# Optimization experiments

Measured on AMD Instinct MI355X. Metric: run time of the kernel, lower is better.

## Reference

```python
import jax, jax.numpy as jnp
import numpy as np

N, H, W, M = 1, 128, 128, 16
HID, STY, CIN, NC, COL = 256, 256, 128, 7, 64


def _lrelu(v):
    return jnp.where(v > 0, v, 0.2 * v)


def _conv(x, w, b=None):
    y = jax.lax.conv_general_dilated(x, w, (1, 1), 'SAME',
                                     dimension_numbers=('NCHW', 'OIHW', 'NCHW'))
    return y if b is None else y + b[None, :, None, None]


def _modlin(f, z, Wt, Wa, ba, Wb, bb):
    # ModLinear, bias=False, mod_bias=True, output_mode=True:
    # y = (f * alpha) @ W^T + beta
    alpha = z @ Wa.T + ba          # [N, in]
    beta = z @ Wb.T + bb           # [N, out]
    return jnp.einsum('nsi,oi->nso', f * alpha[:, None, :], Wt) + beta[:, None, :]


def setup_inputs() -> dict:
    key = jax.random.key(0)
    k = jax.random.split(key, 24)
    s = lambda f: np.float32(1.0 / np.sqrt(f))
    inp = {}
    inp['x'] = jax.random.normal(k[0], (N, H, W, M, CIN), jnp.float32)
    inp['m'] = jax.random.uniform(k[1], (N, H, W, M, NC), jnp.float32)
    inp['z'] = jax.random.normal(k[2], (N, STY), jnp.float32)
    inp['dists'] = jax.random.uniform(k[3], (N, H, W, M), jnp.float32) * 0.05
    # RenderMLP params
    inp['w1'] = jax.random.normal(k[4], (HID, CIN)) * s(CIN)
    inp['b1'] = jnp.zeros((HID,), jnp.float32)
    inp['wma'] = jax.random.normal(k[5], (HID, NC)) * s(NC)
    # 5 stacked ModLinears (fc_2, fc_3, fc_4, fc_5, fc_6)
    inp['ml_w'] = jax.random.normal(k[6], (5, HID, HID)) * s(HID)
    inp['ml_wa'] = jax.random.normal(k[7], (5, HID, STY)) * s(STY)
    inp['ml_ba'] = jnp.ones((5, HID), jnp.float32)
    inp['ml_wb'] = jax.random.normal(k[8], (5, HID, STY)) * s(STY)
    inp['ml_bb'] = jnp.zeros((5, HID), jnp.float32)
    inp['wsig'] = jax.random.normal(k[9], (1, HID)) * s(HID)
    inp['bsig'] = jnp.zeros((1,), jnp.float32)
    inp['wc'] = jax.random.normal(k[10], (COL, HID)) * s(HID)
    inp['bc'] = jnp.zeros((COL,), jnp.float32)
    # RenderCNN params
    inp['wz'] = jax.random.normal(k[11], (4 * HID, STY)) * s(STY)
    inp['bz'] = jnp.zeros((4 * HID,), jnp.float32)
    inp['c1_w'] = jax.random.normal(k[12], (HID, COL, 1, 1)) * s(COL)
    inp['c1_b'] = jnp.zeros((HID,), jnp.float32)
    inp['c2a_w'] = jax.random.normal(k[13], (HID, HID, 3, 3)) * s(HID * 9)
    inp['c2a_b'] = jnp.zeros((HID,), jnp.float32)
    inp['c2b_w'] = jax.random.normal(k[14], (HID, HID, 3, 3)) * s(HID * 9)
    inp['c3a_w'] = jax.random.normal(k[15], (HID, HID, 3, 3)) * s(HID * 9)
    inp['c3a_b'] = jnp.zeros((HID,), jnp.float32)
    inp['c3b_w'] = jax.random.normal(k[16], (HID, HID, 3, 3)) * s(HID * 9)
    inp['c4a_w'] = jax.random.normal(k[17], (HID, HID, 1, 1)) * s(HID)
    inp['c4a_b'] = jnp.zeros((HID,), jnp.float32)
    inp['c4b_w'] = jax.random.normal(k[18], (HID, HID, 1, 1)) * s(HID)
    inp['c4b_b'] = jnp.zeros((HID,), jnp.float32)
    inp['c4_w'] = jax.random.normal(k[19], (3, HID, 1, 1)) * s(HID)
    inp['c4_b'] = jnp.zeros((3,), jnp.float32)
    return inp


def reference(x, m, z, dists, w1, b1, wma, ml_w, ml_wa, ml_ba, ml_wb, ml_bb,
              wsig, bsig, wc, bc, wz, bz, c1_w, c1_b, c2a_w, c2a_b, c2b_w,
              c3a_w, c3a_b, c3b_w, c4a_w, c4a_b, c4b_w, c4b_b, c4_w, c4_b):
    n, h, w_, mm, cin = x.shape
    xf = x.reshape(n, -1, cin)              # [N, S, 128], S = H*W*M
    mf = m.reshape(n, -1, m.shape[-1])      # [N, S, 7]
    # RenderMLP
    f = jnp.einsum('nsi,oi->nso', xf, w1) + b1 + jnp.einsum('nsi,oi->nso', mf, wma)
    f = _lrelu(f)
    for i in range(3):  # fc_2, fc_3, fc_4
        f = _lrelu(_modlin(f, z, ml_w[i], ml_wa[i], ml_ba[i], ml_wb[i], ml_bb[i]))
    sigma = jnp.einsum('nsi,oi->nso', f, wsig) + bsig   # [N, S, 1]
    for i in (3, 4):    # fc_5, fc_6
        f = _lrelu(_modlin(f, z, ml_w[i], ml_wa[i], ml_ba[i], ml_wb[i], ml_bb[i]))
    c = jnp.einsum('nsi,oi->nso', f, wc) + bc           # [N, S, 64]
    # Volumetric alpha compositing along the M ray samples
    sigma = sigma.reshape(n, h, w_, mm)
    c = c.reshape(n, h, w_, mm, -1)
    alpha = 1.0 - jnp.exp(-jax.nn.relu(sigma) * dists)  # [N,H,W,M]
    t = jnp.cumprod(1.0 - alpha + 1e-10, axis=-1)
    t_excl = jnp.concatenate([jnp.ones_like(t[..., :1]), t[..., :-1]], axis=-1)
    wgt = alpha * t_excl
    feat = jnp.einsum('nhwm,nhwmc->nchw', wgt, c)       # [N, 64, H, W]
    # RenderCNN with style modulation
    zc = z @ wz.T + bz
    a0, a1, a2, a3 = jnp.split(zc, 4, axis=-1)
    mod = lambda y, wm, bm: y * (wm[:, :, None, None] + 1.0) + bm[:, :, None, None]
    y = _lrelu(_conv(feat, c1_w, c1_b))
    y = y + _conv(_lrelu(_conv(y, c2a_w, c2a_b)), c2b_w)
    y = _lrelu(mod(y, a0, a1))
    y = y + _conv(_lrelu(_conv(y, c3a_w, c3a_b)), c3b_w)
    y = _lrelu(mod(y, a2, a3))
    y = y + _conv(_lrelu(_conv(y, c4a_w, c4a_b)), c4b_w, c4b_b)
    y = _lrelu(y)
    return _conv(y, c4_w, c4_b)  # [N, 3, H, W]
```

## Files before the change

### kernel.cpp

```cpp
#include <hip/hip_runtime.h>
#include <hip/hip_bf16.h>

#define NPIX 16384
#define S_TOT 262144

typedef __attribute__((ext_vector_type(8))) short bf16x8;
typedef __attribute__((ext_vector_type(4))) float f32x4;

__device__ __forceinline__ float lrelu(float v) { return v > 0.f ? v : 0.2f * v; }
__device__ __forceinline__ unsigned short f2b(float f) {
  unsigned u = __float_as_uint(f);
  return (unsigned short)((u + 0x7FFFu + ((u >> 16) & 1u)) >> 16);
}
__device__ __forceinline__ unsigned pk2(float a, float b) {
  return (unsigned)f2b(a) | ((unsigned)f2b(b) << 16);
}
__device__ __forceinline__ float b2f(short s) {
  return __uint_as_float(((unsigned)(unsigned short)s) << 16);
}
__device__ __forceinline__ float f_lo(int u) { return __uint_as_float((unsigned)u << 16); }
__device__ __forceinline__ float f_hi(int u) { return __uint_as_float((unsigned)u & 0xffff0000u); }

__device__ float g_alpha[5 * 256];
__device__ float g_beta[5 * 256];
__device__ float g_amod[1024];
__device__ float g_sigma[S_TOT];
__device__ float g_c[S_TOT * 64];
__device__ short g_featb[NPIX * 64];
__device__ short g_y1[NPIX * 256];
__device__ short g_y2[NPIX * 256];
__device__ short g_y3[NPIX * 256];
__device__ short g_t [NPIX * 256];
__device__ short g_wpack[385024];
#define O_C1  0
#define O_C2A 16384
#define O_C2B (16384 + 589824)
#define O_C3A (16384 + 2 * 589824)
#define O_C3B (16384 + 3 * 589824)
#define O_C4A (16384 + 4 * 589824)
#define O_C4B (16384 + 4 * 589824 + 65536)
__device__ short g_wpack2[2506752];

__global__ __launch_bounds__(256) void kparams(const float* __restrict__ z,
    const float* __restrict__ wa, const float* __restrict__ ba,
    const float* __restrict__ wb, const float* __restrict__ bb,
    const float* __restrict__ wz, const float* __restrict__ bz) {
  __shared__ float zs[256];
  const int t = threadIdx.x;
  zs[t] = z[t];
  __syncthreads();
  for (int l = 0; l < 5; ++l) {
    float accA = ba[l * 256 + t];
    float accB = bb[l * 256 + t];
    const float* rowA = wa + (l * 256 + t) * 256;
    const float* rowB = wb + (l * 256 + t) * 256;
    for (int k = 0; k < 256; k += 4) {
      float4 va = *(const float4*)(rowA + k);
      float4 vb = *(const float4*)(rowB + k);
      accA += va.x * zs[k] + va.y * zs[k + 1] + va.z * zs[k + 2] + va.w * zs[k + 3];
      accB += vb.x * zs[k] + vb.y * zs[k + 1] + vb.z * zs[k + 2] + vb.w * zs[k + 3];
    }
    g_alpha[l * 256 + t] = accA;
    g_beta[l * 256 + t] = accB;
  }
  for (int j = t; j < 1024; j += 256) {
    float acc = bz[j];
    const float* row = wz + j * 256;
    for (int k = 0; k < 256; k += 4) {
      float4 v = *(const float4*)(row + k);
      acc += v.x * zs[k] + v.y * zs[k + 1] + v.z * zs[k + 2] + v.w * zs[k + 3];
    }
    g_amod[j] = acc;
  }
}

__global__ __launch_bounds__(256) void kprep(
    const float* __restrict__ w1, const float* __restrict__ wma,
    const float* __restrict__ mlw, const float* __restrict__ wc) {
  const int idx = blockIdx.x * 256 + threadIdx.x;
  float val;
  if (idx < 40960) {
    int mt = idx / 2560, r2 = idx % 2560;
    int ks = r2 / 512, r = r2 % 512;
    int ln = r >> 3, j = r & 7;
    int oc = mt * 16 + (ln & 15);
    int k = ks * 32 + (ln >> 4) * 8 + j;
    val = (k < 128) ? w1[oc * 128 + k] : ((k < 135) ? wma[oc * 7 + (k - 128)] : 0.f);
  } else if (idx < 368640) {
    int t = idx - 40960;
    int l = t / 65536, t2 = t % 65536;
    int mt = t2 / 4096, r2 = t2 % 4096;
    int ks = r2 / 512, r = r2 % 512;
    int ln = r >> 3, j = r & 7;
    int oc = mt * 16 + (ln & 15);
    int k = ks * 32 + (ln >> 4) * 8 + j;
    val = mlw[l * 65536 + oc * 256 + k] * g_alpha[l * 256 + k];
  } else {
    int t = idx - 368640;
    int mt = t / 4096, r2 = t % 4096;
    int ks = r2 / 512, r = r2 % 512;
    int ln = r >> 3, j = r & 7;
    int oc = mt * 16 + (ln & 15);
    int k = ks * 32 + (ln >> 4) * 8 + j;
    val = wc[oc * 256 + k];
  }
  g_wpack[idx] = (short)f2b(val);
}

__global__ __launch_bounds__(256) void kprep_cnn(
    const float* __restrict__ c1w,
    const float* __restrict__ c2aw, const float* __restrict__ c2bw,
    const float* __restrict__ c3aw, const float* __restrict__ c3bw,
    const float* __restrict__ c4aw, const float* __restrict__ c4bw) {
  const int idx = blockIdx.x * 256 + threadIdx.x;
  float val;
  if (idx < 16384) {
    int mt = idx / 1024, r2 = idx % 1024;
    int ks = r2 / 512, r = r2 % 512;
    int ln = r >> 3, j = r & 7;
    int oc = mt * 16 + (ln & 15);
    int k = ks * 32 + (ln >> 4) * 8 + j;
    val = c1w[oc * 64 + k];
  } else if (idx < O_C4A) {
    int t = idx - 16384;
    int cv = t / 589824, t2 = t % 589824;
    const float* w = (cv == 0) ? c2aw : (cv == 1) ? c2bw : (cv == 2) ? c3aw : c3bw;
    int mt = t2 / 36864, r2 = t2 % 36864;
    int ks = r2 / 512, r = r2 % 512;
    int ln = r >> 3, j = r & 7;
    int oc = mt * 16 + (ln & 15);
    int k = ks * 32 + (ln >> 4) * 8 + j;
    int tap = k >> 8, ic = k & 255;
    val = w[oc * 2304 + ic * 9 + tap];
  } else {
    int t = idx - O_C4A;
    const float* w = (t < 65536) ? c4aw : c4bw;
    int t2 = t & 65535;
    int mt = t2 / 4096, r2 = t2 % 4096;
    int ks = r2 / 512, r = r2 % 512;
    int ln = r >> 3, j = r & 7;
    int oc = mt * 16 + (ln & 15);
    int k = ks * 32 + (ln >> 4) * 8 + j;
    val = w[oc * 256 + k];
  }
  g_wpack2[idx] = (short)f2b(val);
}

__device__ __forceinline__ bf16x8 ldsB(const short* buf, int s, int kbyte) {
  const char* p = (const char*)buf + s * 512 + (kbyte ^ ((s & 7) << 4));
  return *(const bf16x8*)p;
}

template<int KS>
__device__ __forceinline__ void layer_gemm(const short* __restrict__ gA,
    const short* __restrict__ inb, short* __restrict__ outb,
    const float* __restrict__ bias, int lane, int w) {
  const f32x4 zero = {0.f, 0.f, 0.f, 0.f};
  f32x4 acc[4][4];
#pragma unroll
  for (int mi = 0; mi < 4; ++mi)
#pragma unroll
    for (int ni = 0; ni < 4; ++ni) acc[mi][ni] = zero;
  const int lrow = lane & 15;
  const int lkb = (lane >> 4) * 16;
#pragma unroll
  for (int ks = 0; ks < KS; ++ks) {
    bf16x8 A[4], B[4];
#pragma unroll
    for (int mi = 0; mi < 4; ++mi)
      A[mi] = *(const bf16x8*)(gA + (size_t)((w * 4 + mi) * KS + ks) * 512 + lane * 8);
#pragma unroll
    for (int ni = 0; ni < 4; ++ni)
      B[ni] = ldsB(inb, ni * 16 + lrow, ks * 64 + lkb);
#pragma unroll
    for (int mi = 0; mi < 4; ++mi)
#pragma unroll
      for (int ni = 0; ni < 4; ++ni)
        acc[mi][ni] = __builtin_amdgcn_mfma_f32_16x16x32_bf16(A[mi], B[ni], acc[mi][ni], 0, 0, 0);
  }
  const int rb = (lane >> 4) * 4;
#pragma unroll
  for (int mi = 0; mi < 4; ++mi) {
    const int oc0 = w * 64 + mi * 16 + rb;
    const float b0 = bias[oc0], b1 = bias[oc0 + 1], b2 = bias[oc0 + 2], b3 = bias[oc0 + 3];
#pragma unroll
    for (int ni = 0; ni < 4; ++ni) {
      const int s = ni * 16 + lrow;
      f32x4 a = acc[mi][ni];
      float v0 = lrelu(a[0] + b0), v1 = lrelu(a[1] + b1);
      float v2 = lrelu(a[2] + b2), v3 = lrelu(a[3] + b3);
      char* p = (char*)outb + s * 512 + ((oc0 * 2) ^ ((s & 7) << 4));
      *(int2*)p = make_int2((int)pk2(v0, v1), (int)pk2(v2, v3));
    }
  }
}

__global__ __launch_bounds__(256, 2) void kmlp_mfma(
    const float* __restrict__ x, const float* __restrict__ m_in,
    const float* __restrict__ b1, const float* __restrict__ bc,
    const float* __restrict__ wsig, const float* __restrict__ bsig) {
  __shared__ short fbuf[2][16384];
  __shared__ float bias_all[1600];
  __shared__ float wsig_lds[256];
  __shared__ float sred[256];
  const int tid = threadIdx.x;
  const int lane = tid & 63, w = tid >> 6;
  const int s0 = blockIdx.x * 64;

  {
    const float* xp = x + (size_t)s0 * 128;
    const int s = tid >> 2, c = tid & 3;
#pragma unroll
    for (int e = 0; e < 4; ++e) {
      float4 f0 = *(const float4*)(xp + s * 128 + c * 32 + e * 8);
      float4 f1 = *(const float4*)(xp + s * 128 + c * 32 + e * 8 + 4);
      int4 pk;
      pk.x = (int)pk2(f0.x, f0.y); pk.y = (int)pk2(f0.z, f0.w);
      pk.z = (int)pk2(f1.x, f1.y); pk.w = (int)pk2(f1.z, f1.w);
      char* p = (char*)fbuf[0] + s * 512 + ((c * 64 + e * 16) ^ ((s & 7) << 4));
      *(int4*)p = pk;
    }
  }
  if (tid < 64) {
    const float* mp = m_in + (size_t)(s0 + tid) * 7;
    float mv[8];
#pragma unroll
    for (int q = 0; q < 7; ++q) mv[q] = mp[q];
    mv[7] = 0.f;
    int4 pk;
    pk.x = (int)pk2(mv[0], mv[1]); pk.y = (int)pk2(mv[2], mv[3]);
    pk.z = (int)pk2(mv[4], mv[5]); pk.w = (int)pk2(mv[6], mv[7]);
    char* base = (char*)fbuf[0] + tid * 512;
    const int swz = (tid & 7) << 4;
    *(int4*)(base + (256 ^ swz)) = pk;
    int4 zz = make_int4(0, 0, 0, 0);
    *(int4*)(base + (272 ^ swz)) = zz;
    *(int4*)(base + (288 ^ swz)) = zz;
    *(int4*)(base + (304 ^ swz)) = zz;
  }
  bias_all[tid] = b1[tid];
  for (int i = tid; i < 1280; i += 256) bias_all[256 + i] = g_beta[i];
  if (tid < 64) bias_all[1536 + tid] = bc[tid];
  wsig_lds[tid] = wsig[tid];
  __syncthreads();

  layer_gemm<5>(g_wpack,                     fbuf[0], fbuf[1], bias_all,        lane, w);
  __syncthreads();
  layer_gemm<8>(g_wpack + 40960,             fbuf[1], fbuf[0], bias_all + 256,  lane, w);
  __syncthreads();
  layer_gemm<8>(g_wpack + 40960 + 65536,     fbuf[0], fbuf[1], bias_all + 512,  lane, w);
  __syncthreads();
  layer_gemm<8>(g_wpack + 40960 + 2 * 65536, fbuf[1], fbuf[0], bias_all + 768,  lane, w);
  __syncthreads();
  {
    const int s = tid & 63, q = tid >> 6;
    float part = 0.f;
#pragma unroll
    for (int e = 0; e < 8; ++e) {
      bf16x8 v = ldsB(fbuf[0], s, q * 128 + e * 16);
      const float* wp = wsig_lds + q * 64 + e * 8;
#pragma unroll
      for (int j = 0; j < 8; ++j) part += b2f(v[j]) * wp[j];
    }
    sred[q * 64 + s] = part;
  }
  __syncthreads();
  if (tid < 64)
    g_sigma[s0 + tid] = sred[tid] + sred[64 + tid] + sred[128 + tid] + sred[192 + tid] + bsig[0];
  layer_gemm<8>(g_wpack + 40960 + 3 * 65536, fbuf[0], fbuf[1], bias_all + 1024, lane, w);
  __syncthreads();
  layer_gemm<8>(g_wpack + 40960 + 4 * 65536, fbuf[1], fbuf[0], bias_all + 1280, lane, w);
  __syncthreads();
  {
    const f32x4 zero = {0.f, 0.f, 0.f, 0.f};
    f32x4 acc[4] = {zero, zero, zero, zero};
    const int lrow = lane & 15, lkb = (lane >> 4) * 16;
    const short* gA = g_wpack + 368640;
#pragma unroll
    for (int ks = 0; ks < 8; ++ks) {
      bf16x8 A = *(const bf16x8*)(gA + (size_t)(w * 8 + ks) * 512 + lane * 8);
#pragma unroll
      for (int ni = 0; ni < 4; ++ni) {
        bf16x8 B = ldsB(fbuf[0], ni * 16 + lrow, ks * 64 + lkb);
        acc[ni] = __builtin_amdgcn_mfma_f32_16x16x32_bf16(A, B, acc[ni], 0, 0, 0);
      }
    }
    const int rb = (lane >> 4) * 4;
    const int oc0 = w * 16 + rb;
    const float b0 = bias_all[1536 + oc0], b1v = bias_all[1537 + oc0];
    const float b2v = bias_all[1538 + oc0], b3 = bias_all[1539 + oc0];
#pragma unroll
    for (int ni = 0; ni < 4; ++ni) {
      const int s = ni * 16 + lrow;
      float4 vv;
      vv.x = acc[ni][0] + b0; vv.y = acc[ni][1] + b1v;
      vv.z = acc[ni][2] + b2v; vv.w = acc[ni][3] + b3;
      *(float4*)(g_c + (size_t)(s0 + s) * 64 + oc0) = vv;
    }
  }
}

__global__ __launch_bounds__(256) void kcomposite(const float* __restrict__ dists) {
  const int tid = threadIdx.x;
  const int p = blockIdx.x * 4 + (tid >> 6);
  const int ch = tid & 63;
  const int base = p * 16;
  float T = 1.f, acc = 0.f;
  for (int mm = 0; mm < 16; ++mm) {
    float sgm = g_sigma[base + mm];
    float d = dists[base + mm];
    float a = 1.f - expf(-fmaxf(sgm, 0.f) * d);
    acc += a * T * g_c[(size_t)(base + mm) * 64 + ch];
    T *= (1.f - a + 1e-10f);
  }
  g_featb[p * 64 + ch] = (short)f2b(acc);
}

template<int IC>
__global__ __launch_bounds__(256, 2) void kgemm1x1(const short* __restrict__ in,
    const short* __restrict__ gA, const float* __restrict__ bias,
    const short* __restrict__ res, int domod, const float* __restrict__ modAB,
    short* __restrict__ out) {
  constexpr int KS = IC / 32;
  constexpr int ROWB = IC * 2;
  __shared__ short binb[32 * IC];
  const int tid = threadIdx.x;
  const int lane = tid & 63, w = tid >> 6;
  const int px0 = blockIdx.x * 32;

  for (int e = tid; e < 32 * IC / 8; e += 256) {
    const int px = e / (IC / 8), lg = e % (IC / 8);
    bf16x8 v = *(const bf16x8*)(in + (size_t)(px0 + px) * IC + lg * 8);
    char* p = (char*)binb + px * ROWB + ((lg * 16) ^ ((px & 7) << 4));
    *(bf16x8*)p = v;
  }
  __syncthreads();

  const f32x4 zero = {0.f, 0.f, 0.f, 0.f};
  f32x4 acc[4][2];
#pragma unroll
  for (int mi = 0; mi < 4; ++mi)
#pragma unroll
    for (int ni = 0; ni < 2; ++ni) acc[mi][ni] = zero;
  const int lrow = lane & 15;
  const int lkb = (lane >> 4) * 16;
#pragma unroll
  for (int ks = 0; ks < KS; ++ks) {
    bf16x8 A[4], B[2];
#pragma unroll
    for (int mi = 0; mi < 4; ++mi)
      A[mi] = *(const bf16x8*)(gA + (size_t)((w * 4 + mi) * KS + ks) * 512 + lane * 8);
#pragma unroll
    for (int ni = 0; ni < 2; ++ni) {
      const int s = ni * 16 + lrow;
      const char* p = (const char*)binb + s * ROWB + ((ks * 64 + lkb) ^ ((s & 7) << 4));
      B[ni] = *(const bf16x8*)p;
    }
#pragma unroll
    for (int mi = 0; mi < 4; ++mi)
#pragma unroll
      for (int ni = 0; ni < 2; ++ni)
        acc[mi][ni] = __builtin_amdgcn_mfma_f32_16x16x32_bf16(A[mi], B[ni], acc[mi][ni], 0, 0, 0);
  }
  const int rb = (lane >> 4) * 4;
#pragma unroll
  for (int mi = 0; mi < 4; ++mi) {
    const int oc = w * 64 + mi * 16 + rb;
    float bv[4] = {0.f, 0.f, 0.f, 0.f};
    if (bias) { bv[0] = bias[oc]; bv[1] = bias[oc + 1]; bv[2] = bias[oc + 2]; bv[3] = bias[oc + 3]; }
#pragma unroll
    for (int ni = 0; ni < 2; ++ni) {
      const int gpx = px0 + ni * 16 + lrow;
      f32x4 a = acc[mi][ni];
      float v[4];
#pragma unroll
      for (int r = 0; r < 4; ++r) v[r] = a[r] + bv[r];
      if (res) {
        int2 rv = *(const int2*)(res + (size_t)gpx * 256 + oc);
        v[0] += f_lo(rv.x); v[1] += f_hi(rv.x); v[2] += f_lo(rv.y); v[3] += f_hi(rv.y);
      }
      if (domod) {
#pragma unroll
        for (int r = 0; r < 4; ++r) v[r] = v[r] * (modAB[oc + r] + 1.f) + modAB[256 + oc + r];
      }
#pragma unroll
      for (int r = 0; r < 4; ++r) v[r] = lrelu(v[r]);
      *(int2*)(out + (size_t)gpx * 256 + oc) = make_int2((int)pk2(v[0], v[1]), (int)pk2(v[2], v[3]));
    }
  }
}

__global__ __launch_bounds__(256, 2) void kconv3(const short* __restrict__ in,
    const short* __restrict__ gA, const float* __restrict__ bias,
    const short* __restrict__ res, int domod, const float* __restrict__ modAB,
    short* __restrict__ out) {
  __shared__ short halo[136 * 64];
  const int tid = threadIdx.x;
  const int lane = tid & 63, w = tid >> 6;
  const int oct = blockIdx.x >> 8;
  const int pxt = blockIdx.x & 255;
  const int x0 = (pxt & 3) * 32, y0 = (pxt >> 2) * 2;
  const int oc0 = oct * 128 + w * 32;
  const int lrow = lane & 15;
  const int lkb = (lane >> 4) * 16;

  const f32x4 zero = {0.f, 0.f, 0.f, 0.f};
  f32x4 acc[2][4];
#pragma unroll
  for (int mi = 0; mi < 2; ++mi)
#pragma unroll
    for (int ni = 0; ni < 4; ++ni) acc[mi][ni] = zero;

#pragma unroll 1
  for (int c = 0; c < 4; ++c) {
    for (int e = tid; e < 1088; e += 256) {
      const int row = e >> 3, lg = e & 7;
      const int yy = row / 34, xx = row - yy * 34;
      const int gy = y0 - 1 + yy, gx = x0 - 1 + xx;
      bf16x8 v = {0, 0, 0, 0, 0, 0, 0, 0};
      if (gy >= 0 && gy < 128 && gx >= 0 && gx < 128)
        v = *(const bf16x8*)(in + (size_t)((gy << 7) + gx) * 256 + c * 64 + lg * 8);
      char* p = (char*)halo + row * 128 + ((lg * 16) ^ ((row & 7) << 4));
      *(bf16x8*)p = v;
    }
    __syncthreads();
#pragma unroll
    for (int tap = 0; tap < 9; ++tap) {
      const int ky = tap / 3, kx = tap - ky * 3;
#pragma unroll
      for (int s = 0; s < 2; ++s) {
        const int ksg = tap * 8 + c * 2 + s;
        bf16x8 A[2], B[4];
#pragma unroll
        for (int mi = 0; mi < 2; ++mi)
          A[mi] = *(const bf16x8*)(gA + (size_t)(((oct * 8 + w * 2 + mi) * 72 + ksg)) * 512 + lane * 8);
#pragma unroll
        for (int ni = 0; ni < 4; ++ni) {
          const int p = ni * 16 + lrow;
          const int row = ((p >> 5) + ky) * 34 + (p & 31) + kx;
          const char* bp = (const char*)halo + row * 128 + ((s * 64 + lkb) ^ ((row & 7) << 4));
          B[ni] = *(const bf16x8*)bp;
        }
#pragma unroll
        for (int mi = 0; mi < 2; ++mi)
#pragma unroll
          for (int ni = 0; ni < 4; ++ni)
            acc[mi][ni] = __builtin_amdgcn_mfma_f32_16x16x32_bf16(A[mi], B[ni], acc[mi][ni], 0, 0, 0);
      }
    }
    __syncthreads();
  }

  const int rb = (lane >> 4) * 4;
#pragma unroll
  for (int mi = 0; mi < 2; ++mi) {
    const int oc = oc0 + mi * 16 + rb;
    float bv[4] = {0.f, 0.f, 0.f, 0.f};
    if (bias) { bv[0] = bias[oc]; bv[1] = bias[oc + 1]; bv[2] = bias[oc + 2]; bv[3] = bias[oc + 3]; }
#pragma unroll
    for (int ni = 0; ni < 4; ++ni) {
      const int p = ni * 16 + lrow;
      const int gpx = (y0 + (p >> 5)) * 128 + x0 + (p & 31);
      f32x4 a = acc[mi][ni];
      float v[4];
#pragma unroll
      for (int r = 0; r < 4; ++r) v[r] = a[r] + bv[r];
      if (res) {
        int2 rv = *(const int2*)(res + (size_t)gpx * 256 + oc);
        v[0] += f_lo(rv.x); v[1] += f_hi(rv.x); v[2] += f_lo(rv.y); v[3] += f_hi(rv.y);
      }
      if (domod) {
#pragma unroll
        for (int r = 0; r < 4; ++r) v[r] = v[r] * (modAB[oc + r] + 1.f) + modAB[256 + oc + r];
      }
#pragma unroll
      for (int r = 0; r < 4; ++r) v[r] = lrelu(v[r]);
      *(int2*)(out + (size_t)gpx * 256 + oc) = make_int2((int)pk2(v[0], v[1]), (int)pk2(v[2], v[3]));
    }
  }
}

__global__ __launch_bounds__(256) void kfinal(const short* __restrict__ in,
    const float* __restrict__ w, const float* __restrict__ bias, float* __restrict__ outp) {
  __shared__ float wl[768];
  const int tid = threadIdx.x;
  for (int i = tid; i < 768; i += 256) wl[i] = w[i];
  __syncthreads();
  const int lane = tid & 63;
  const int px = blockIdx.x * 8 + (tid >> 6) * 2 + (lane >> 5);
  const int j = lane & 31;
  bf16x8 v = *(const bf16x8*)(in + (size_t)px * 256 + j * 8);
  float s0 = 0.f, s1 = 0.f, s2 = 0.f;
#pragma unroll
  for (int q = 0; q < 8; ++q) {
    float f = b2f(v[q]);
    s0 += f * wl[j * 8 + q];
    s1 += f * wl[256 + j * 8 + q];
    s2 += f * wl[512 + j * 8 + q];
  }
#pragma unroll
  for (int off = 1; off < 32; off <<= 1) {
    s0 += __shfl_xor(s0, off);
    s1 += __shfl_xor(s1, off);
    s2 += __shfl_xor(s2, off);
  }
  if (j == 0) {
    outp[px] = s0 + bias[0];
    outp[NPIX + px] = s1 + bias[1];
    outp[2 * NPIX + px] = s2 + bias[2];
  }
}

extern "C" void kernel_launch(void* const* d_in, const int* in_sizes, int n_in,
                              void* d_out, int out_size, void* d_ws, size_t ws_size,
                              hipStream_t stream) {
  (void)in_sizes; (void)n_in; (void)out_size; (void)d_ws; (void)ws_size;
  const float* x    = (const float*)d_in[0];
  const float* m    = (const float*)d_in[1];
  const float* z    = (const float*)d_in[2];
  const float* dists= (const float*)d_in[3];
  const float* w1   = (const float*)d_in[4];
  const float* b1   = (const float*)d_in[5];
  const float* wma  = (const float*)d_in[6];
  const float* mlw  = (const float*)d_in[7];
  const float* mlwa = (const float*)d_in[8];
  const float* mlba = (const float*)d_in[9];
  const float* mlwb = (const float*)d_in[10];
  const float* mlbb = (const float*)d_in[11];
  const float* wsig = (const float*)d_in[12];
  const float* bsig = (const float*)d_in[13];
  const float* wc   = (const float*)d_in[14];
  const float* bc   = (const float*)d_in[15];
  const float* wz   = (const float*)d_in[16];
  const float* bz   = (const float*)d_in[17];
  const float* c1w  = (const float*)d_in[18];
  const float* c1b  = (const float*)d_in[19];
  const float* c2aw = (const float*)d_in[20];
  const float* c2ab = (const float*)d_in[21];
  const float* c2bw = (const float*)d_in[22];
  const float* c3aw = (const float*)d_in[23];
  const float* c3ab = (const float*)d_in[24];
  const float* c3bw = (const float*)d_in[25];
  const float* c4aw = (const float*)d_in[26];
  const float* c4ab = (const float*)d_in[27];
  const float* c4bw = (const float*)d_in[28];
  const float* c4bb = (const float*)d_in[29];
  const float* c4w  = (const float*)d_in[30];
  const float* c4b  = (const float*)d_in[31];
  float* outp = (float*)d_out;

  short *pW2, *pFb, *pY1, *pY2, *pY3, *pT;
  float *pAmod;
  hipGetSymbolAddress((void**)&pW2, HIP_SYMBOL(g_wpack2));
  hipGetSymbolAddress((void**)&pFb, HIP_SYMBOL(g_featb));
  hipGetSymbolAddress((void**)&pY1, HIP_SYMBOL(g_y1));
  hipGetSymbolAddress((void**)&pY2, HIP_SYMBOL(g_y2));
  hipGetSymbolAddress((void**)&pY3, HIP_SYMBOL(g_y3));
  hipGetSymbolAddress((void**)&pT,  HIP_SYMBOL(g_t));
  hipGetSymbolAddress((void**)&pAmod, HIP_SYMBOL(g_amod));

  kparams<<<1, 256, 0, stream>>>(z, mlwa, mlba, mlwb, mlbb, wz, bz);
  kprep<<<1504, 256, 0, stream>>>(w1, wma, mlw, wc);
  kprep_cnn<<<9792, 256, 0, stream>>>(c1w, c2aw, c2bw, c3aw, c3bw, c4aw, c4bw);
  kmlp_mfma<<<4096, 256, 0, stream>>>(x, m, b1, bc, wsig, bsig);
  kcomposite<<<4096, 256, 0, stream>>>(dists);
  kgemm1x1<64> <<<512, 256, 0, stream>>>(pFb, pW2 + O_C1,  c1b,  nullptr, 0, nullptr, pY1);
  kconv3<<<512, 256, 0, stream>>>(pY1, pW2 + O_C2A, c2ab, nullptr, 0, nullptr,      pT);
  kconv3<<<512, 256, 0, stream>>>(pT,  pW2 + O_C2B, nullptr, pY1, 1, pAmod,         pY2);
  kconv3<<<512, 256, 0, stream>>>(pY2, pW2 + O_C3A, c3ab, nullptr, 0, nullptr,      pT);
  kconv3<<<512, 256, 0, stream>>>(pT,  pW2 + O_C3B, nullptr, pY2, 1, pAmod + 512,   pY3);
  kgemm1x1<256><<<512, 256, 0, stream>>>(pY3, pW2 + O_C4A, c4ab, nullptr, 0, nullptr, pT);
  kgemm1x1<256><<<512, 256, 0, stream>>>(pT,  pW2 + O_C4B, c4bb, pY3,    0, nullptr, pY1);
  kfinal<<<2048, 256, 0, stream>>>(pY1, c4w, c4b, outp);
}
```

Measured before the change: 632.1 us.

## Restructure MLP kernel so each wave owns 64 samples with register-resident activations

The fused MLP kernel now gives each wave its own 64-sample tile in a private LDS buffer, so the block-wide __syncthreads between layers go away. Each wave loads its input fragments into registers once per layer and loops over all 16 output tiles, double-buffering weight fragments read from global memory. The sigma head becomes an MFMA against a zero-padded packed wsig instead of a scalar reduction, and the biases are precomputed into one global array. In exchange each wave streams the whole weight matrix by itself, and register pressure and the use of 128KB LDS per block limit occupancy to one block.

```diff
diff --git a/kernel.cpp b/kernel.cpp
--- a/kernel.cpp
+++ b/kernel.cpp
@@ -22,7 +22,7 @@
 __device__ __forceinline__ float f_hi(int u) { return __uint_as_float((unsigned)u & 0xffff0000u); }
 
 __device__ float g_alpha[5 * 256];
-__device__ float g_beta[5 * 256];
+__device__ float g_biasall[1600];
 __device__ float g_amod[1024];
 __device__ float g_sigma[S_TOT];
 __device__ float g_c[S_TOT * 64];
@@ -31,7 +31,7 @@
 __device__ short g_y2[NPIX * 256];
 __device__ short g_y3[NPIX * 256];
 __device__ short g_t [NPIX * 256];
-__device__ short g_wpack[385024];
+__device__ short g_wpack[389120];
 #define O_C1  0
 #define O_C2A 16384
 #define O_C2B (16384 + 589824)
@@ -44,11 +44,14 @@
 __global__ __launch_bounds__(256) void kparams(const float* __restrict__ z,
     const float* __restrict__ wa, const float* __restrict__ ba,
     const float* __restrict__ wb, const float* __restrict__ bb,
-    const float* __restrict__ wz, const float* __restrict__ bz) {
+    const float* __restrict__ wz, const float* __restrict__ bz,
+    const float* __restrict__ b1, const float* __restrict__ bc) {
   __shared__ float zs[256];
   const int t = threadIdx.x;
   zs[t] = z[t];
   __syncthreads();
+  g_biasall[t] = b1[t];
+  if (t < 64) g_biasall[1536 + t] = bc[t];
   for (int l = 0; l < 5; ++l) {
     float accA = ba[l * 256 + t];
     float accB = bb[l * 256 + t];
@@ -61,7 +64,7 @@
       accB += vb.x * zs[k] + vb.y * zs[k + 1] + vb.z * zs[k + 2] + vb.w * zs[k + 3];
     }
     g_alpha[l * 256 + t] = accA;
-    g_beta[l * 256 + t] = accB;
+    g_biasall[256 + l * 256 + t] = accB;
   }
   for (int j = t; j < 1024; j += 256) {
     float acc = bz[j];
@@ -76,7 +79,8 @@
 
 __global__ __launch_bounds__(256) void kprep(
     const float* __restrict__ w1, const float* __restrict__ wma,
-    const float* __restrict__ mlw, const float* __restrict__ wc) {
+    const float* __restrict__ mlw, const float* __restrict__ wc,
+    const float* __restrict__ wsig) {
   const int idx = blockIdx.x * 256 + threadIdx.x;
   float val;
   if (idx < 40960) {
@@ -95,7 +99,7 @@
     int oc = mt * 16 + (ln & 15);
     int k = ks * 32 + (ln >> 4) * 8 + j;
     val = mlw[l * 65536 + oc * 256 + k] * g_alpha[l * 256 + k];
-  } else {
+  } else if (idx < 385024) {
     int t = idx - 368640;
     int mt = t / 4096, r2 = t % 4096;
     int ks = r2 / 512, r = r2 % 512;
@@ -103,6 +107,13 @@
     int oc = mt * 16 + (ln & 15);
     int k = ks * 32 + (ln >> 4) * 8 + j;
     val = wc[oc * 256 + k];
+  } else {
+    int t = idx - 385024;
+    int ks = t / 512, r = t % 512;
+    int ln = r >> 3, j = r & 7;
+    int row = ln & 15;
+    int k = ks * 32 + (ln >> 4) * 8 + j;
+    val = (row == 0) ? wsig[k] : 0.f;
   }
   g_wpack[idx] = (short)f2b(val);
 }
@@ -150,152 +161,160 @@
   const char* p = (const char*)buf + s * 512 + (kbyte ^ ((s & 7) << 4));
   return *(const bf16x8*)p;
 }
+__device__ __forceinline__ bf16x8 ldA(const short* gA, int frag, int lane) {
+  return *(const bf16x8*)(gA + ((size_t)frag << 9) + lane * 8);
+}
 
 template<int KS>
-__device__ __forceinline__ void layer_gemm(const short* __restrict__ gA,
-    const short* __restrict__ inb, short* __restrict__ outb,
-    const float* __restrict__ bias, int lane, int w) {
+__device__ __forceinline__ void refill(const short* fb, bf16x8 (&bin)[4][8], int lane) {
+  const int lrow = lane & 15, lkb = (lane >> 4) * 16;
+#pragma unroll
+  for (int ni = 0; ni < 4; ++ni)
+#pragma unroll
+    for (int ks = 0; ks < KS; ++ks)
+      bin[ni][ks] = ldsB(fb, ni * 16 + lrow, ks * 64 + lkb);
+}
+
+template<int KS>
+__device__ __forceinline__ void mt_proc(const bf16x8 (&A)[8], const bf16x8 (&bin)[4][8],
+    const float* __restrict__ gbias, short* fb, int mt, int lane) {
   const f32x4 zero = {0.f, 0.f, 0.f, 0.f};
-  f32x4 acc[4][4];
-#pragma unroll
-  for (int mi = 0; mi < 4; ++mi)
-#pragma unroll
-    for (int ni = 0; ni < 4; ++ni) acc[mi][ni] = zero;
-  const int lrow = lane & 15;
-  const int lkb = (lane >> 4) * 16;
-#pragma unroll
-  for (int ks = 0; ks < KS; ++ks) {
-    bf16x8 A[4], B[4];
-#pragma unroll
-    for (int mi = 0; mi < 4; ++mi)
-      A[mi] = *(const bf16x8*)(gA + (size_t)((w * 4 + mi) * KS + ks) * 512 + lane * 8);
+  f32x4 acc[4] = {zero, zero, zero, zero};
+#pragma unroll
+  for (int ks = 0; ks < KS; ++ks)
 #pragma unroll
     for (int ni = 0; ni < 4; ++ni)
-      B[ni] = ldsB(inb, ni * 16 + lrow, ks * 64 + lkb);
-#pragma unroll
-    for (int mi = 0; mi < 4; ++mi)
-#pragma unroll
-      for (int ni = 0; ni < 4; ++ni)
-        acc[mi][ni] = __builtin_amdgcn_mfma_f32_16x16x32_bf16(A[mi], B[ni], acc[mi][ni], 0, 0, 0);
-  }
-  const int rb = (lane >> 4) * 4;
-#pragma unroll
-  for (int mi = 0; mi < 4; ++mi) {
-    const int oc0 = w * 64 + mi * 16 + rb;
-    const float b0 = bias[oc0], b1 = bias[oc0 + 1], b2 = bias[oc0 + 2], b3 = bias[oc0 + 3];
-#pragma unroll
-    for (int ni = 0; ni < 4; ++ni) {
-      const int s = ni * 16 + lrow;
-      f32x4 a = acc[mi][ni];
-      float v0 = lrelu(a[0] + b0), v1 = lrelu(a[1] + b1);
-      float v2 = lrelu(a[2] + b2), v3 = lrelu(a[3] + b3);
-      char* p = (char*)outb + s * 512 + ((oc0 * 2) ^ ((s & 7) << 4));
-      *(int2*)p = make_int2((int)pk2(v0, v1), (int)pk2(v2, v3));
-    }
-  }
-}
-
-__global__ __launch_bounds__(256, 2) void kmlp_mfma(
+      acc[ni] = __builtin_amdgcn_mfma_f32_16x16x32_bf16(A[ks], bin[ni][ks], acc[ni], 0, 0, 0);
+  const int lrow = lane & 15, q = lane >> 4;
+  const f32x4 bv = *(const f32x4*)(gbias + mt * 16 + q * 4);
+  const int oc0 = mt * 16 + q * 4;
+#pragma unroll
+  for (int ni = 0; ni < 4; ++ni) {
+    const int s = ni * 16 + lrow;
+    float v0 = lrelu(acc[ni][0] + bv[0]), v1 = lrelu(acc[ni][1] + bv[1]);
+    float v2 = lrelu(acc[ni][2] + bv[2]), v3 = lrelu(acc[ni][3] + bv[3]);
+    char* p = (char*)fb + s * 512 + ((oc0 * 2) ^ ((s & 7) << 4));
+    *(int2*)p = make_int2((int)pk2(v0, v1), (int)pk2(v2, v3));
+  }
+}
+
+template<int KS>
+__device__ __forceinline__ void gemm_layer(const short* __restrict__ gA,
+    const float* __restrict__ gbias, bf16x8 (&bin)[4][8], short* fb, int lane) {
+  bf16x8 A0[8], A1[8];
+#pragma unroll
+  for (int ks = 0; ks < KS; ++ks) A0[ks] = ldA(gA, 0 * KS + ks, lane);
+#pragma unroll 1
+  for (int mt = 0; mt < 16; mt += 2) {
+#pragma unroll
+    for (int ks = 0; ks < KS; ++ks) A1[ks] = ldA(gA, (mt + 1) * KS + ks, lane);
+    mt_proc<KS>(A0, bin, gbias, fb, mt, lane);
+    const int mtn = (mt + 2 < 16) ? mt + 2 : 0;
+#pragma unroll
+    for (int ks = 0; ks < KS; ++ks) A0[ks] = ldA(gA, mtn * KS + ks, lane);
+    mt_proc<KS>(A1, bin, gbias, fb, mt + 1, lane);
+  }
+}
+
+__global__ __launch_bounds__(256, 1) void kmlp_reg(
     const float* __restrict__ x, const float* __restrict__ m_in,
-    const float* __restrict__ b1, const float* __restrict__ bc,
-    const float* __restrict__ wsig, const float* __restrict__ bsig) {
-  __shared__ short fbuf[2][16384];
-  __shared__ float bias_all[1600];
-  __shared__ float wsig_lds[256];
-  __shared__ float sred[256];
+    const float* __restrict__ bsig) {
+  __shared__ __align__(16) short fbuf[4][16384];
   const int tid = threadIdx.x;
   const int lane = tid & 63, w = tid >> 6;
-  const int s0 = blockIdx.x * 64;
+  const int s0 = (blockIdx.x * 4 + w) * 64;
+  short* fb = fbuf[w];
+  const int lrow = lane & 15, q = lane >> 4;
 
   {
     const float* xp = x + (size_t)s0 * 128;
-    const int s = tid >> 2, c = tid & 3;
-#pragma unroll
-    for (int e = 0; e < 4; ++e) {
-      float4 f0 = *(const float4*)(xp + s * 128 + c * 32 + e * 8);
-      float4 f1 = *(const float4*)(xp + s * 128 + c * 32 + e * 8 + 4);
+#pragma unroll 1
+    for (int i = 0; i < 16; ++i) {
+      const int e = i * 64 + lane;
+      const int row = e >> 4, c8 = e & 15;
+      float4 f0 = *(const float4*)(xp + row * 128 + c8 * 8);
+      float4 f1 = *(const float4*)(xp + row * 128 + c8 * 8 + 4);
       int4 pk;
       pk.x = (int)pk2(f0.x, f0.y); pk.y = (int)pk2(f0.z, f0.w);
       pk.z = (int)pk2(f1.x, f1.y); pk.w = (int)pk2(f1.z, f1.w);
-      char* p = (char*)fbuf[0] + s * 512 + ((c * 64 + e * 16) ^ ((s & 7) << 4));
+      char* p = (char*)fb + row * 512 + ((c8 * 16) ^ ((row & 7) << 4));
       *(int4*)p = pk;
     }
   }
-  if (tid < 64) {
-    const float* mp = m_in + (size_t)(s0 + tid) * 7;
+  {
+    const float* mp = m_in + (size_t)(s0 + lane) * 7;
     float mv[8];
 #pragma unroll
-    for (int q = 0; q < 7; ++q) mv[q] = mp[q];
+    for (int qq = 0; qq < 7; ++qq) mv[qq] = mp[qq];
     mv[7] = 0.f;
     int4 pk;
     pk.x = (int)pk2(mv[0], mv[1]); pk.y = (int)pk2(mv[2], mv[3]);
     pk.z = (int)pk2(mv[4], mv[5]); pk.w = (int)pk2(mv[6], mv[7]);
-    char* base = (char*)fbuf[0] + tid * 512;
-    const int swz = (tid & 7) << 4;
-    *(int4*)(base + (256 ^ swz)) = pk;
+    char* base = (char*)fb + lane * 512;
+    const int sw = (lane & 7) << 4;
+    *(int4*)(base + (256 ^ sw)) = pk;
     int4 zz = make_int4(0, 0, 0, 0);
-    *(int4*)(base + (272 ^ swz)) = zz;
-    *(int4*)(base + (288 ^ swz)) = zz;
-    *(int4*)(base + (304 ^ swz)) = zz;
-  }
-  bias_all[tid] = b1[tid];
-  for (int i = tid; i < 1280; i += 256) bias_all[256 + i] = g_beta[i];
-  if (tid < 64) bias_all[1536 + tid] = bc[tid];
-  wsig_lds[tid] = wsig[tid];
-  __syncthreads();
-
-  layer_gemm<5>(g_wpack,                     fbuf[0], fbuf[1], bias_all,        lane, w);
-  __syncthreads();
-  layer_gemm<8>(g_wpack + 40960,             fbuf[1], fbuf[0], bias_all + 256,  lane, w);
-  __syncthreads();
-  layer_gemm<8>(g_wpack + 40960 + 65536,     fbuf[0], fbuf[1], bias_all + 512,  lane, w);
-  __syncthreads();
-  layer_gemm<8>(g_wpack + 40960 + 2 * 65536, fbuf[1], fbuf[0], bias_all + 768,  lane, w);
-  __syncthreads();
-  {
-    const int s = tid & 63, q = tid >> 6;
-    float part = 0.f;
-#pragma unroll
-    for (int e = 0; e < 8; ++e) {
-      bf16x8 v = ldsB(fbuf[0], s, q * 128 + e * 16);
-      const float* wp = wsig_lds + q * 64 + e * 8;
-#pragma unroll
-      for (int j = 0; j < 8; ++j) part += b2f(v[j]) * wp[j];
-    }
-    sred[q * 64 + s] = part;
-  }
-  __syncthreads();
-  if (tid < 64)
-    g_sigma[s0 + tid] = sred[tid] + sred[64 + tid] + sred[128 + tid] + sred[192 + tid] + bsig[0];
-  layer_gemm<8>(g_wpack + 40960 + 3 * 65536, fbuf[0], fbuf[1], bias_all + 1024, lane, w);
-  __syncthreads();
-  layer_gemm<8>(g_wpack + 40960 + 4 * 65536, fbuf[1], fbuf[0], bias_all + 1280, lane, w);
-  __syncthreads();
+    *(int4*)(base + (272 ^ sw)) = zz;
+    *(int4*)(base + (288 ^ sw)) = zz;
+    *(int4*)(base + (304 ^ sw)) = zz;
+  }
+
+  bf16x8 bin[4][8];
+  refill<5>(fb, bin, lane);
+  gemm_layer<5>(g_wpack, g_biasall, bin, fb, lane);
+  refill<8>(fb, bin, lane);
+  gemm_layer<8>(g_wpack + 40960, g_biasall + 256, bin, fb, lane);
+  refill<8>(fb, bin, lane);
+  gemm_layer<8>(g_wpack + 40960 + 65536, g_biasall + 512, bin, fb, lane);
+  refill<8>(fb, bin, lane);
+  gemm_layer<8>(g_wpack + 40960 + 131072, g_biasall + 768, bin, fb, lane);
+  refill<8>(fb, bin, lane);
   {
     const f32x4 zero = {0.f, 0.f, 0.f, 0.f};
-    f32x4 acc[4] = {zero, zero, zero, zero};
-    const int lrow = lane & 15, lkb = (lane >> 4) * 16;
-    const short* gA = g_wpack + 368640;
+    f32x4 sacc[4] = {zero, zero, zero, zero};
+    const short* gS = g_wpack + 385024;
 #pragma unroll
     for (int ks = 0; ks < 8; ++ks) {
-      bf16x8 A = *(const bf16x8*)(gA + (size_t)(w * 8 + ks) * 512 + lane * 8);
+      bf16x8 A = ldA(gS, ks, lane);
+#pragma unroll
+      for (int ni = 0; ni < 4; ++ni)
+        sacc[ni] = __builtin_amdgcn_mfma_f32_16x16x32_bf16(A, bin[ni][ks], sacc[ni], 0, 0, 0);
+    }
+    const float b0 = bsig[0];
+    if (lane < 16) {
+#pragma unroll
+      for (int ni = 0; ni < 4; ++ni)
+        g_sigma[s0 + ni * 16 + lane] = sacc[ni][0] + b0;
+    }
+  }
+  gemm_layer<8>(g_wpack + 40960 + 196608, g_biasall + 1024, bin, fb, lane);
+  refill<8>(fb, bin, lane);
+  gemm_layer<8>(g_wpack + 40960 + 262144, g_biasall + 1280, bin, fb, lane);
+  refill<8>(fb, bin, lane);
+  {
+    const short* gC = g_wpack + 368640;
+#pragma unroll 1
+    for (int mt = 0; mt < 4; ++mt) {
+      const f32x4 zero = {0.f, 0.f, 0.f, 0.f};
+      f32x4 acc[4] = {zero, zero, zero, zero};
+      bf16x8 A[8];
+#pragma unroll
+      for (int ks = 0; ks < 8; ++ks) A[ks] = ldA(gC, mt * 8 + ks, lane);
+#pragma unroll
+      for (int ks = 0; ks < 8; ++ks)
+#pragma unroll
+        for (int ni = 0; ni < 4; ++ni)
+          acc[ni] = __builtin_amdgcn_mfma_f32_16x16x32_bf16(A[ks], bin[ni][ks], acc[ni], 0, 0, 0);
+      const int oc0 = mt * 16 + q * 4;
+      const f32x4 bv = *(const f32x4*)(g_biasall + 1536 + oc0);
 #pragma unroll
       for (int ni = 0; ni < 4; ++ni) {
-        bf16x8 B = ldsB(fbuf[0], ni * 16 + lrow, ks * 64 + lkb);
-        acc[ni] = __builtin_amdgcn_mfma_f32_16x16x32_bf16(A, B, acc[ni], 0, 0, 0);
+        const int s = ni * 16 + lrow;
+        float4 vv;
+        vv.x = acc[ni][0] + bv[0]; vv.y = acc[ni][1] + bv[1];
+        vv.z = acc[ni][2] + bv[2]; vv.w = acc[ni][3] + bv[3];
+        *(float4*)(g_c + (size_t)(s0 + s) * 64 + oc0) = vv;
       }
-    }
-    const int rb = (lane >> 4) * 4;
-    const int oc0 = w * 16 + rb;
-    const float b0 = bias_all[1536 + oc0], b1v = bias_all[1537 + oc0];
-    const float b2v = bias_all[1538 + oc0], b3 = bias_all[1539 + oc0];
-#pragma unroll
-    for (int ni = 0; ni < 4; ++ni) {
-      const int s = ni * 16 + lrow;
-      float4 vv;
-      vv.x = acc[ni][0] + b0; vv.y = acc[ni][1] + b1v;
-      vv.z = acc[ni][2] + b2v; vv.w = acc[ni][3] + b3;
-      *(float4*)(g_c + (size_t)(s0 + s) * 64 + oc0) = vv;
     }
   }
 }
@@ -559,10 +578,10 @@
   hipGetSymbolAddress((void**)&pT,  HIP_SYMBOL(g_t));
   hipGetSymbolAddress((void**)&pAmod, HIP_SYMBOL(g_amod));
 
-  kparams<<<1, 256, 0, stream>>>(z, mlwa, mlba, mlwb, mlbb, wz, bz);
-  kprep<<<1504, 256, 0, stream>>>(w1, wma, mlw, wc);
+  kparams<<<1, 256, 0, stream>>>(z, mlwa, mlba, mlwb, mlbb, wz, bz, b1, bc);
+  kprep<<<1520, 256, 0, stream>>>(w1, wma, mlw, wc, wsig);
   kprep_cnn<<<9792, 256, 0, stream>>>(c1w, c2aw, c2bw, c3aw, c3bw, c4aw, c4bw);
-  kmlp_mfma<<<4096, 256, 0, stream>>>(x, m, b1, bc, wsig, bsig);
+  kmlp_reg<<<1024, 256, 0, stream>>>(x, m, bsig);
   kcomposite<<<4096, 256, 0, stream>>>(dists);
   kgemm1x1<64> <<<512, 256, 0, stream>>>(pFb, pW2 + O_C1,  c1b,  nullptr, 0, nullptr, pY1);
   kconv3<<<512, 256, 0, stream>>>(pY1, pW2 + O_C2A, c2ab, nullptr, 0, nullptr,      pT);
```

Result: slower. 685.0 us (+8.4%).
